# Optimization experiments

Measured on AMD Instinct MI355X. Metric: run time of the kernel, lower is better.

Reference implementation:

```python
import jax, jax.numpy as jnp
import numpy as np


def _conv2d_valid(x, w):
    # x: (N, C, H, W), w: (O, C, kH, kW) -> (N, O, H-kH+1, W-kW+1)
    return jax.lax.conv_general_dilated(
        x, w, window_strides=(1, 1), padding='VALID',
        dimension_numbers=('NCHW', 'OIHW', 'NCHW'))


def setup_inputs() -> dict:
    key = jax.random.key(0)
    kx, ky = jax.random.split(key)
    x = jax.random.normal(kx, (16, 64, 128, 128), dtype=jnp.float32)
    y = jax.random.normal(ky, (64, 64, 16, 16), dtype=jnp.float32)
    return {"x": x, "y": y}


def reference(x, y):
    # Normalize each of the K kernels to unit L2 norm (sum over C, kH, kW).
    normed_y = y / jnp.sqrt(jnp.sum(y * y, axis=(1, 2, 3), keepdims=True))
    # Per-window L2 norm of x via ones-kernel box conv over x^2.
    ones_kernel = jnp.ones(y.shape, dtype=x.dtype)
    x_norm = jnp.sqrt(_conv2d_valid(x * x, ones_kernel))
    # Normalized cross-correlation, clamped at zero.
    diss = _conv2d_valid(x, normed_y) / x_norm
    return jax.nn.relu(diss)
```

## Files before the change

### kernel.cpp

```cpp
#include <hip/hip_runtime.h>
#include <stdint.h>

#define GAS __attribute__((address_space(1)))
#define LAS __attribute__((address_space(3)))

typedef __attribute__((ext_vector_type(8))) short short8;
typedef __attribute__((ext_vector_type(4))) float float4v;
typedef __attribute__((ext_vector_type(4))) unsigned int uint4v;

__device__ __forceinline__ unsigned short f2bf(float f) {
  union { float f; unsigned int u; } v; v.f = f;
  unsigned int r = v.u + 0x7fffu + ((v.u >> 16) & 1u);
  return (unsigned short)(r >> 16);
}

__device__ __forceinline__ void async_g2l16(const void* g, void* l) {
  __builtin_amdgcn_global_load_lds((const GAS unsigned int*)g,
                                   (LAS unsigned int*)l, 16, 0, 0);
}

__device__ __forceinline__ void vmem_drain() {
  asm volatile("s_waitcnt vmcnt(0)" ::: "memory");
}

__global__ void knorm_y(const float* __restrict__ y, unsigned short* __restrict__ y_t2) {
  int o = blockIdx.x;
  int tid = threadIdx.x;
  const float* yo = y + o * 16384;
  float s = 0.f;
  for (int idx = tid; idx < 16384; idx += 256) { float v = yo[idx]; s += v * v; }
  for (int off = 32; off; off >>= 1) s += __shfl_down(s, off, 64);
  __shared__ float red[4];
  if ((tid & 63) == 0) red[tid >> 6] = s;
  __syncthreads();
  float rn = 1.0f / sqrtf(red[0] + red[1] + red[2] + red[3]);
  int og = o >> 4, ol = o & 15;
  for (int idx = tid; idx < 16384; idx += 256) {
    int c = idx >> 8, dy = (idx >> 4) & 15, dx = idx & 15;
    int t = dy * 16 + dx;
    int cb = c >> 5, q = (c >> 3) & 3, j = c & 7;
    size_t dst = (size_t)t * 4096 + (size_t)(og * 2 + cb) * 512 + (q * 16 + ol) * 8 + j;
    y_t2[dst] = f2bf(yo[idx] * rn);
  }
}

__global__ void ktrans_x(const float* __restrict__ x, unsigned short* __restrict__ x_t,
                         float* __restrict__ s) {
  int h = blockIdx.x, n = blockIdx.y;
  int tid = threadIdx.x;
  __shared__ __align__(16) unsigned short tb[8192];
  __shared__ float sb[256];
  const float* xb = x + ((size_t)n * 64) * 16384 + h * 128;
  int w = tid & 127, half = tid >> 7;
  float acc = 0.f;
#pragma unroll
  for (int cs = 0; cs < 4; ++cs) {
    short8 tmp;
#pragma unroll
    for (int j = 0; j < 8; ++j) {
      int c = half * 32 + cs * 8 + j;
      float v = xb[(size_t)c * 16384 + w];
      tmp[j] = (short)f2bf(v);
      acc += v * v;
    }
    int chunk = (half * 4 + cs) ^ (w & 7);
    *(short8*)(tb + w * 64 + chunk * 8) = tmp;
  }
  sb[tid] = acc;
  __syncthreads();
  uint4v* dst = (uint4v*)(x_t + ((size_t)(n * 128 + h)) * 8192);
  const uint4v* src = (const uint4v*)tb;
  for (int idx = tid; idx < 1024; idx += 256) dst[idx] = src[idx];
  if (tid < 128) s[((size_t)(n * 128 + h)) * 128 + tid] = sb[tid] + sb[tid + 128];
}

__global__ void knorm_x(const float* __restrict__ s, float* __restrict__ invn) {
  int i = blockIdx.x, n = blockIdx.y;
  int tid = threadIdx.x;
  __shared__ float colsum[128];
  const float* sp = s + ((size_t)(n * 128 + i)) * 128;
  float a = 0.f;
#pragma unroll
  for (int dy = 0; dy < 16; ++dy) a += sp[dy * 128 + tid];
  colsum[tid] = a;
  __syncthreads();
  if (tid < 113) {
    float acc = 0.f;
#pragma unroll
    for (int dx = 0; dx < 16; ++dx) acc += colsum[tid + dx];
    invn[((size_t)n * 113 + i) * 113 + tid] = 1.0f / sqrtf(acc);
  }
}

__launch_bounds__(256, 4)
__global__ void kconv(const unsigned short* __restrict__ x_t,
                      const unsigned short* __restrict__ y_t2,
                      const float* __restrict__ invn,
                      float* __restrict__ out) {
  int i = blockIdx.x;
  int n = blockIdx.y;
  int tid = threadIdx.x;
  int lane = tid & 63, wave = tid >> 6;
  int lane15 = lane & 15, q = lane >> 4;
  int wrow = wave >> 1, wcol = wave & 1;

  __shared__ __align__(16) char smem[32768];
  char* const A0 = smem;
  char* const A1 = smem + 16384;

  const char* xrow0 = (const char*)(x_t + ((size_t)(n * 128 + i)) * 8192);

  auto stageA = [&](int dy, char* buf) {
    const char* src = xrow0 + (size_t)dy * 16384;
#pragma unroll
    for (int it = 0; it < 4; ++it) {
      int chunk = it * 256 + wave * 64;
      async_g2l16(src + (chunk + lane) * 16, buf + chunk * 16);
    }
  };

  const short8* ybase = (const short8*)(y_t2 + (size_t)wcol * 2048 + (size_t)lane * 8);
  auto loadB = [&](int t, short8 bf[2][2]) {
    const short8* p = ybase + (size_t)t * 512;
    bf[0][0] = p[0];
    bf[0][1] = p[64];
    bf[1][0] = p[128];
    bf[1][1] = p[192];
  };

  float4v acc[4][2];
#pragma unroll
  for (int mt = 0; mt < 4; ++mt)
#pragma unroll
    for (int nt = 0; nt < 2; ++nt) acc[mt][nt] = (float4v){0.f, 0.f, 0.f, 0.f};

  int abase[4];
#pragma unroll
  for (int mt = 0; mt < 4; ++mt) abase[mt] = (wrow * 64 + mt * 16 + lane15) * 128;

  short8 b0[2][2], b1[2][2];
  stageA(0, A0);
  loadB(0, b0);
  vmem_drain();
  __syncthreads();

#pragma unroll 1
  for (int dy = 0; dy < 16; ++dy) {
    char* Ab = (dy & 1) ? A1 : A0;
    if (dy < 15) {
      __builtin_amdgcn_sched_barrier(0);
      stageA(dy + 1, (dy & 1) ? A0 : A1);
      __builtin_amdgcn_sched_barrier(0);
    }
#pragma unroll
    for (int dx = 0; dx < 16; ++dx) {
      int t = dy * 16 + dx;
      short8(&bc)[2][2] = (dx & 1) ? b1 : b0;
      short8(&bn)[2][2] = (dx & 1) ? b0 : b1;
      if (t < 255) loadB(t + 1, bn);
      int xr = (lane15 + dx) & 7;
#pragma unroll
      for (int cb = 0; cb < 2; ++cb) {
        int aoff = dx * 128 + (((q + cb * 4) ^ xr) << 4);
#pragma unroll
        for (int mt = 0; mt < 4; ++mt) {
          short8 a = *(const short8*)(Ab + abase[mt] + aoff);
          acc[mt][0] = __builtin_amdgcn_mfma_f32_16x16x32_bf16(a, bc[0][cb], acc[mt][0], 0, 0, 0);
          acc[mt][1] = __builtin_amdgcn_mfma_f32_16x16x32_bf16(a, bc[1][cb], acc[mt][1], 0, 0, 0);
        }
      }
    }
    asm volatile("s_waitcnt vmcnt(4)" ::: "memory");
    __syncthreads();
  }

  float* cs = (float*)smem;
  float* ivs = cs + 4352;
  const float* ivp = invn + ((size_t)n * 113 + i) * 113;
  if (tid < 128) ivs[tid] = (tid < 113) ? ivp[tid] : 0.f;
  float* op = out + (size_t)n * 64 * 12769 + (size_t)i * 113;
#pragma unroll 1
  for (int p = 0; p < 2; ++p) {
    if (wcol == p) {
#pragma unroll
      for (int mt = 0; mt < 4; ++mt)
#pragma unroll
        for (int nt = 0; nt < 2; ++nt) {
          int row = nt * 16 + lane15;
          int j0 = wrow * 64 + mt * 16 + q * 4;
          *(float4v*)(cs + row * 132 + j0) = acc[mt][nt];
        }
    }
    __syncthreads();
    for (int idx = tid; idx < 4096; idx += 256) {
      int o2 = idx >> 7, j = idx & 127;
      if (j < 113) {
        float v = cs[o2 * 132 + j] * ivs[j];
        op[(size_t)(p * 32 + o2) * 12769 + j] = fmaxf(v, 0.f);
      }
    }
    __syncthreads();
  }
}

extern "C" void kernel_launch(void* const* d_in, const int* in_sizes, int n_in,
                              void* d_out, int out_size, void* d_ws, size_t ws_size,
                              hipStream_t stream) {
  const float* x = (const float*)d_in[0];
  const float* y = (const float*)d_in[1];
  float* out = (float*)d_out;
  char* ws = (char*)d_ws;
  unsigned short* x_t = (unsigned short*)ws;
  unsigned short* y_t2 = (unsigned short*)(ws + 33554432);
  float* s = (float*)(ws + 35651584);
  float* invn = (float*)(ws + 36700160);

  hipLaunchKernelGGL(knorm_y, dim3(64), dim3(256), 0, stream, y, y_t2);
  hipLaunchKernelGGL(ktrans_x, dim3(128, 16), dim3(256), 0, stream, x, x_t, s);
  hipLaunchKernelGGL(knorm_x, dim3(113, 16), dim3(128), 0, stream, s, invn);
  hipLaunchKernelGGL(kconv, dim3(113, 16), dim3(256), 0, stream, x_t, y_t2, invn, out);
}
```

Measured before the change: 533.2 us.

## Give each wave all 64 output channels and store the epilogue straight from registers

The conv kernel drops from four waves in a 2x2 split to two waves per block. Each wave now covers 64 output columns and all 64 kernels with a 4x4 grid of MFMA tiles, so every A fragment read from LDS feeds four MFMAs instead of two. The epilogue no longer stages through LDS with extra barriers. It applies the inverse norm and ReLU in registers and writes float4 values to global memory, with special handling for the last column. The cost is more registers per wave (64 accumulators plus double-buffered B), fewer waves per block, and unaligned strided float4 global stores.

```diff
diff --git a/kernel.cpp b/kernel.cpp
--- a/kernel.cpp
+++ b/kernel.cpp
@@ -92,7 +92,7 @@
   }
 }
 
-__launch_bounds__(256, 4)
+__launch_bounds__(128, 2)
 __global__ void kconv(const unsigned short* __restrict__ x_t,
                       const unsigned short* __restrict__ y_t2,
                       const float* __restrict__ invn,
@@ -102,7 +102,6 @@
   int tid = threadIdx.x;
   int lane = tid & 63, wave = tid >> 6;
   int lane15 = lane & 15, q = lane >> 4;
-  int wrow = wave >> 1, wcol = wave & 1;
 
   __shared__ __align__(16) char smem[32768];
   char* const A0 = smem;
@@ -113,32 +112,33 @@
   auto stageA = [&](int dy, char* buf) {
     const char* src = xrow0 + (size_t)dy * 16384;
 #pragma unroll
-    for (int it = 0; it < 4; ++it) {
-      int chunk = it * 256 + wave * 64;
+    for (int it = 0; it < 8; ++it) {
+      int chunk = it * 128 + wave * 64;
       async_g2l16(src + (chunk + lane) * 16, buf + chunk * 16);
     }
   };
 
-  const short8* ybase = (const short8*)(y_t2 + (size_t)wcol * 2048 + (size_t)lane * 8);
-  auto loadB = [&](int t, short8 bf[2][2]) {
+  const short8* ybase = (const short8*)y_t2 + lane;
+  auto loadB = [&](int t, short8 bf[4][2]) {
     const short8* p = ybase + (size_t)t * 512;
-    bf[0][0] = p[0];
-    bf[0][1] = p[64];
-    bf[1][0] = p[128];
-    bf[1][1] = p[192];
+#pragma unroll
+    for (int nt = 0; nt < 4; ++nt) {
+      bf[nt][0] = p[nt * 128];
+      bf[nt][1] = p[nt * 128 + 64];
+    }
   };
 
-  float4v acc[4][2];
+  float4v acc[4][4];
 #pragma unroll
   for (int mt = 0; mt < 4; ++mt)
 #pragma unroll
-    for (int nt = 0; nt < 2; ++nt) acc[mt][nt] = (float4v){0.f, 0.f, 0.f, 0.f};
+    for (int nt = 0; nt < 4; ++nt) acc[mt][nt] = (float4v){0.f, 0.f, 0.f, 0.f};
 
   int abase[4];
 #pragma unroll
-  for (int mt = 0; mt < 4; ++mt) abase[mt] = (wrow * 64 + mt * 16 + lane15) * 128;
-
-  short8 b0[2][2], b1[2][2];
+  for (int mt = 0; mt < 4; ++mt) abase[mt] = (wave * 64 + mt * 16 + lane15) * 128;
+
+  short8 b0[4][2], b1[4][2];
   stageA(0, A0);
   loadB(0, b0);
   vmem_drain();
@@ -155,8 +155,8 @@
 #pragma unroll
     for (int dx = 0; dx < 16; ++dx) {
       int t = dy * 16 + dx;
-      short8(&bc)[2][2] = (dx & 1) ? b1 : b0;
-      short8(&bn)[2][2] = (dx & 1) ? b0 : b1;
+      short8(&bc)[4][2] = (dx & 1) ? b1 : b0;
+      short8(&bn)[4][2] = (dx & 1) ? b0 : b1;
       if (t < 255) loadB(t + 1, bn);
       int xr = (lane15 + dx) & 7;
 #pragma unroll
@@ -165,41 +165,43 @@
 #pragma unroll
         for (int mt = 0; mt < 4; ++mt) {
           short8 a = *(const short8*)(Ab + abase[mt] + aoff);
-          acc[mt][0] = __builtin_amdgcn_mfma_f32_16x16x32_bf16(a, bc[0][cb], acc[mt][0], 0, 0, 0);
-          acc[mt][1] = __builtin_amdgcn_mfma_f32_16x16x32_bf16(a, bc[1][cb], acc[mt][1], 0, 0, 0);
+#pragma unroll
+          for (int nt = 0; nt < 4; ++nt)
+            acc[mt][nt] = __builtin_amdgcn_mfma_f32_16x16x32_bf16(a, bc[nt][cb], acc[mt][nt], 0, 0, 0);
         }
       }
     }
-    asm volatile("s_waitcnt vmcnt(4)" ::: "memory");
+    asm volatile("s_waitcnt vmcnt(8)" ::: "memory");
     __syncthreads();
   }
 
-  float* cs = (float*)smem;
-  float* ivs = cs + 4352;
   const float* ivp = invn + ((size_t)n * 113 + i) * 113;
-  if (tid < 128) ivs[tid] = (tid < 113) ? ivp[tid] : 0.f;
   float* op = out + (size_t)n * 64 * 12769 + (size_t)i * 113;
-#pragma unroll 1
-  for (int p = 0; p < 2; ++p) {
-    if (wcol == p) {
-#pragma unroll
-      for (int mt = 0; mt < 4; ++mt)
-#pragma unroll
-        for (int nt = 0; nt < 2; ++nt) {
-          int row = nt * 16 + lane15;
-          int j0 = wrow * 64 + mt * 16 + q * 4;
-          *(float4v*)(cs + row * 132 + j0) = acc[mt][nt];
-        }
-    }
-    __syncthreads();
-    for (int idx = tid; idx < 4096; idx += 256) {
-      int o2 = idx >> 7, j = idx & 127;
-      if (j < 113) {
-        float v = cs[o2 * 132 + j] * ivs[j];
-        op[(size_t)(p * 32 + o2) * 12769 + j] = fmaxf(v, 0.f);
+  int jbase = wave * 64 + q * 4;
+#pragma unroll
+  for (int mt = 0; mt < 4; ++mt) {
+    int j0 = jbase + mt * 16;
+    if (j0 <= 108) {
+      float4v iv = *(const float4v*)(ivp + j0);
+#pragma unroll
+      for (int nt = 0; nt < 4; ++nt) {
+        int o = nt * 16 + lane15;
+        float4v v = acc[mt][nt];
+        float4v r;
+        r[0] = fmaxf(v[0] * iv[0], 0.f);
+        r[1] = fmaxf(v[1] * iv[1], 0.f);
+        r[2] = fmaxf(v[2] * iv[2], 0.f);
+        r[3] = fmaxf(v[3] * iv[3], 0.f);
+        *(float4v*)(op + (size_t)o * 12769 + j0) = r;
       }
-    }
-    __syncthreads();
+    } else if (j0 == 112) {
+      float ivs = ivp[112];
+#pragma unroll
+      for (int nt = 0; nt < 4; ++nt) {
+        int o = nt * 16 + lane15;
+        op[(size_t)o * 12769 + 112] = fmaxf(acc[mt][nt][0] * ivs, 0.f);
+      }
+    }
   }
 }
 
@@ -218,5 +220,5 @@
   hipLaunchKernelGGL(knorm_y, dim3(64), dim3(256), 0, stream, y, y_t2);
   hipLaunchKernelGGL(ktrans_x, dim3(128, 16), dim3(256), 0, stream, x, x_t, s);
   hipLaunchKernelGGL(knorm_x, dim3(113, 16), dim3(128), 0, stream, s, invn);
-  hipLaunchKernelGGL(kconv, dim3(113, 16), dim3(256), 0, stream, x_t, y_t2, invn, out);
-}
+  hipLaunchKernelGGL(kconv, dim3(113, 16), dim3(128), 0, stream, x_t, y_t2, invn, out);
+}
```

Result: slower. 561.9 us (+5.4%).
